# Kernel tuning notes

Hardware: AMD Instinct MI355X
Metric: run time of the kernel (lower is better)

## Reference

```python
import jax, jax.numpy as jnp
import numpy as np

EPS = 1e-12

def _l2norm(v, axis):
    return v / jnp.maximum(jnp.linalg.norm(v, axis=axis, keepdims=True), EPS)

def setup_inputs() -> dict:
    key = jax.random.key(0)
    k1, k2, k3 = jax.random.split(key, 3)
    B, D, C = 65536, 768, 100
    P = C * (C - 1) // 2  # 4950 pairwise local heads
    x = jax.random.normal(k1, (B, D), dtype=jnp.float32)
    first_out = jax.random.normal(k2, (B, C), dtype=jnp.float32)
    weights = jax.random.normal(k3, (P, 2, D), dtype=jnp.float32) * (1.0 / np.sqrt(D))
    sigma = jnp.ones((P,), dtype=jnp.float32)
    return {"x": x, "first_out": first_out, "weights": weights, "sigma": sigma, "cur_stage": 4}

def reference(x, first_out, weights, sigma, cur_stage):
    # top-2 class indices per sample, sorted ascending -> pair key (a, b), a < b
    _, top2 = jax.lax.top_k(first_out, 2)              # [B, 2]
    sorted_idx = jnp.sort(top2, axis=1)                # [B, 2]
    a = sorted_idx[:, 0]
    b = sorted_idx[:, 1]
    pair_idx = b * (b - 1) // 2 + a                    # key 'a-b' -> flat head index
    W = weights[pair_idx]                              # [B, 2, D] gathered expert weights
    s = sigma[pair_idx]                                # [B]
    # CosineLinear (use_RP=False): sigma * normalize(x) @ normalize(W)^T
    xn = _l2norm(x, axis=1)                            # [B, D]
    Wn = _l2norm(W, axis=2)                            # [B, 2, D]
    logits = s[:, None] * jnp.einsum('bd,bkd->bk', xn, Wn)  # [B, 2]
    # pick which of the two candidate classes the local head prefers
    sel = jnp.argmax(logits, axis=1)                   # [B]
    preds = jnp.take_along_axis(sorted_idx, sel[:, None], axis=1)[:, 0]  # [B]
    return preds, logits
```

## Files before the change

### kernel.cpp

```cpp
#include <hip/hip_runtime.h>
#include <math.h>


#define D_DIM 768
#define C_DIM 100
#define EPS_N 1e-12

typedef float vf4 __attribute__((ext_vector_type(4)));

#define ROW_SHR1    0x111
#define ROW_SHR2    0x112
#define ROW_SHR4    0x114
#define ROW_SHR8    0x118
#define ROW_BCAST15 0x142
#define ROW_BCAST31 0x143

template <int CTRL>
__device__ __forceinline__ float dpp0_f32(float v) {
    return __builtin_bit_cast(float, __builtin_amdgcn_update_dpp(
        0, __builtin_bit_cast(int, v), CTRL, 0xF, 0xF, true));
}

template <int CTRL>
__device__ __forceinline__ double dpp0_f64(double v) {
    union { double d; unsigned long long u; } x; x.d = v;
    int lo = (int)(unsigned int)(x.u & 0xffffffffull);
    int hi = (int)(unsigned int)(x.u >> 32);
    int olo = __builtin_amdgcn_update_dpp(0, lo, CTRL, 0xF, 0xF, true);
    int ohi = __builtin_amdgcn_update_dpp(0, hi, CTRL, 0xF, 0xF, true);
    union { unsigned long long u; double d; } y;
    y.u = ((unsigned long long)(unsigned int)ohi << 32) | (unsigned int)olo;
    return y.d;
}

__device__ __forceinline__ float wave_sum_f32(float v) {
    v += dpp0_f32<ROW_SHR1>(v);
    v += dpp0_f32<ROW_SHR2>(v);
    v += dpp0_f32<ROW_SHR4>(v);
    v += dpp0_f32<ROW_SHR8>(v);
    v += dpp0_f32<ROW_BCAST15>(v);
    v += dpp0_f32<ROW_BCAST31>(v);
    return v;
}

__device__ __forceinline__ double wave_sum_f64(double v) {
    v += dpp0_f64<ROW_SHR1>(v);
    v += dpp0_f64<ROW_SHR2>(v);
    v += dpp0_f64<ROW_SHR4>(v);
    v += dpp0_f64<ROW_SHR8>(v);
    v += dpp0_f64<ROW_BCAST15>(v);
    v += dpp0_f64<ROW_BCAST31>(v);
    return v;
}

__device__ __forceinline__ bool vi_gt(float v0, int i0, float v1, int i1) {
    return (v0 > v1) || (v0 == v1 && i0 < i1);
}

template <int CTRL>
__device__ __forceinline__ void t2_step(float& v1, int& i1, float& v2, int& i2) {
    const int NEGINF = 0xFF800000;
    const int BIGIDX = 0x7fffffff;
    float ov1 = __builtin_bit_cast(float, __builtin_amdgcn_update_dpp(
        NEGINF, __builtin_bit_cast(int, v1), CTRL, 0xF, 0xF, false));
    int   oi1 = __builtin_amdgcn_update_dpp(BIGIDX, i1, CTRL, 0xF, 0xF, false);
    float ov2 = __builtin_bit_cast(float, __builtin_amdgcn_update_dpp(
        NEGINF, __builtin_bit_cast(int, v2), CTRL, 0xF, 0xF, false));
    int   oi2 = __builtin_amdgcn_update_dpp(BIGIDX, i2, CTRL, 0xF, 0xF, false);
    if (vi_gt(ov1, oi1, v1, i1)) {
        float nv2; int ni2;
        if (vi_gt(v1, i1, ov2, oi2)) { nv2 = v1;  ni2 = i1; }
        else                         { nv2 = ov2; ni2 = oi2; }
        v1 = ov1; i1 = oi1; v2 = nv2; i2 = ni2;
    } else {
        if (vi_gt(ov1, oi1, v2, i2)) { v2 = ov1; i2 = oi1; }
    }
}

__global__ __launch_bounds__(256) void mlcl_kernel(
    const float* __restrict__ x,
    const float* __restrict__ first_out,
    const float* __restrict__ weights,
    const float* __restrict__ sigma,
    float* __restrict__ out,
    int B)
{
    const int lane = threadIdx.x & 63;
    const int r = (blockIdx.x << 2) + (threadIdx.x >> 6);
    if (r >= B) return;

    const float* fo = first_out + (size_t)r * C_DIM;
    float e0 = fo[lane];
    int   j1 = lane + 64;
    float e1 = (j1 < C_DIM) ? fo[j1] : -INFINITY;

    float v1, v2; int i1, i2;
    if (vi_gt(e1, j1, e0, lane)) { v1 = e1; i1 = j1;   v2 = e0; i2 = lane; }
    else                         { v1 = e0; i1 = lane; v2 = e1; i2 = j1; }

    t2_step<ROW_SHR1>(v1, i1, v2, i2);
    t2_step<ROW_SHR2>(v1, i1, v2, i2);
    t2_step<ROW_SHR4>(v1, i1, v2, i2);
    t2_step<ROW_SHR8>(v1, i1, v2, i2);
    t2_step<ROW_BCAST15>(v1, i1, v2, i2);
    t2_step<ROW_BCAST31>(v1, i1, v2, i2);
    const int gi1 = __builtin_amdgcn_readlane(i1, 63);
    const int gi2 = __builtin_amdgcn_readlane(i2, 63);
    const int a = min(gi1, gi2);
    const int b = max(gi1, gi2);
    const int p = b * (b - 1) / 2 + a;

    const float sig = sigma[p];

    const vf4* xv = (const vf4*)(x + (size_t)r * D_DIM);
    const vf4* wv = (const vf4*)(weights + (size_t)p * (2 * D_DIM));

    vf4 xa0 = xv[lane],       xa1 = xv[lane + 64],       xa2 = xv[lane + 128];
    vf4 w00 = wv[lane],       w01 = wv[lane + 64],       w02 = wv[lane + 128];
    vf4 w10 = wv[192 + lane], w11 = wv[192 + lane + 64], w12 = wv[192 + lane + 128];

    float  xx = 0.f;
    double d0 = 0.0, d1 = 0.0, n0 = 0.0, n1 = 0.0;
#define ACC(xa, w0, w1)                                                       \
    xx += xa.x * xa.x + xa.y * xa.y + xa.z * xa.z + xa.w * xa.w;              \
    d0 += (double)xa.x * w0.x + (double)xa.y * w0.y                           \
        + (double)xa.z * w0.z + (double)xa.w * w0.w;                          \
    d1 += (double)xa.x * w1.x + (double)xa.y * w1.y                           \
        + (double)xa.z * w1.z + (double)xa.w * w1.w;                          \
    n0 += (double)w0.x * w0.x + (double)w0.y * w0.y                           \
        + (double)w0.z * w0.z + (double)w0.w * w0.w;                          \
    n1 += (double)w1.x * w1.x + (double)w1.y * w1.y                           \
        + (double)w1.z * w1.z + (double)w1.w * w1.w;
    ACC(xa0, w00, w10)
    ACC(xa1, w01, w11)
    ACC(xa2, w02, w12)
#undef ACC

    xx = wave_sum_f32(xx);
    d0 = wave_sum_f64(d0);
    d1 = wave_sum_f64(d1);
    n0 = wave_sum_f64(n0);
    n1 = wave_sum_f64(n1);

    if (lane == 63) {
        const double s   = (double)sig;
        const double inx = s / fmax(sqrt((double)xx), EPS_N);
        const double l0  = inx * d0 / fmax(sqrt(n0), EPS_N);
        const double l1  = inx * d1 / fmax(sqrt(n1), EPS_N);
        const int sel = (l1 > l0) ? 1 : 0;
        out[r] = (float)(sel ? b : a);
        float2 lg = make_float2((float)l0, (float)l1);
        *(float2*)(out + B + 2 * (size_t)r) = lg;
    }
}

extern "C" void kernel_launch(void* const* d_in, const int* in_sizes, int n_in,
                              void* d_out, int out_size, void* d_ws, size_t ws_size,
                              hipStream_t stream) {
    const float* x         = (const float*)d_in[0];
    const float* first_out = (const float*)d_in[1];
    const float* weights   = (const float*)d_in[2];
    const float* sigma     = (const float*)d_in[3];
    float* out = (float*)d_out;

    const int B = in_sizes[0] / D_DIM;
    hipLaunchKernelGGL(mlcl_kernel, dim3((B + 3) / 4), dim3(256), 0, stream,
                       x, first_out, weights, sigma, out, B);
}
```

Baseline: 318.4 us.

## Precompute per-head weight inverse norms and process two rows per wavefront

Adds a pre-pass kernel that computes sigma divided by the L2 norm of each of the 9900 weight rows once, in double, and writes the results to workspace. The main kernel then skips the per-sample weight-norm accumulation and reductions and reads two precomputed scalars instead. Each 32-lane half-wave now handles one sample, so reductions are one DPP step shorter, and the x loads are issued before the top-2 search to overlap their latency. The cost is an extra kernel launch and a pass over the weights, plus more registers per lane for the wider per-thread loads.

New measurement: 337.0 us. +5.9%, slower.

```diff
diff --git a/kernel.cpp b/kernel.cpp
--- a/kernel.cpp
+++ b/kernel.cpp
@@ -33,16 +33,22 @@
     return y.d;
 }
 
-__device__ __forceinline__ float wave_sum_f32(float v) {
+__device__ __forceinline__ float half_sum_f32(float v) {
     v += dpp0_f32<ROW_SHR1>(v);
     v += dpp0_f32<ROW_SHR2>(v);
     v += dpp0_f32<ROW_SHR4>(v);
     v += dpp0_f32<ROW_SHR8>(v);
     v += dpp0_f32<ROW_BCAST15>(v);
-    v += dpp0_f32<ROW_BCAST31>(v);
     return v;
 }
-
+__device__ __forceinline__ double half_sum_f64(double v) {
+    v += dpp0_f64<ROW_SHR1>(v);
+    v += dpp0_f64<ROW_SHR2>(v);
+    v += dpp0_f64<ROW_SHR4>(v);
+    v += dpp0_f64<ROW_SHR8>(v);
+    v += dpp0_f64<ROW_BCAST15>(v);
+    return v;
+}
 __device__ __forceinline__ double wave_sum_f64(double v) {
     v += dpp0_f64<ROW_SHR1>(v);
     v += dpp0_f64<ROW_SHR2>(v);
@@ -55,6 +61,12 @@
 
 __device__ __forceinline__ bool vi_gt(float v0, int i0, float v1, int i1) {
     return (v0 > v1) || (v0 == v1 && i0 < i1);
+}
+
+__device__ __forceinline__ void push2(float& v1, int& i1, float& v2, int& i2,
+                                      float v, int i) {
+    if (vi_gt(v, i, v1, i1)) { v2 = v1; i2 = i1; v1 = v; i1 = i; }
+    else if (vi_gt(v, i, v2, i2)) { v2 = v; i2 = i; }
 }
 
 template <int CTRL>
@@ -77,76 +89,112 @@
     }
 }
 
+__global__ __launch_bounds__(256) void norm_kernel(
+    const float* __restrict__ weights,
+    const float* __restrict__ sigma,
+    double* __restrict__ q,
+    int P2)
+{
+    const int lane = threadIdx.x & 63;
+    const int t = (blockIdx.x << 2) + (threadIdx.x >> 6);
+    if (t >= P2) return;
+
+    const vf4* wv = (const vf4*)(weights + (size_t)t * D_DIM);
+    vf4 a0 = wv[lane], a1 = wv[lane + 64], a2 = wv[lane + 128];
+
+    double n = 0.0;
+#define SQ(a)                                                                  \
+    n += (double)a.x * a.x + (double)a.y * a.y                                 \
+       + (double)a.z * a.z + (double)a.w * a.w;
+    SQ(a0) SQ(a1) SQ(a2)
+#undef SQ
+    n = wave_sum_f64(n);
+    if (lane == 63) {
+        q[t] = (double)sigma[t >> 1] / fmax(sqrt(n), EPS_N);
+    }
+}
+
 __global__ __launch_bounds__(256) void mlcl_kernel(
     const float* __restrict__ x,
     const float* __restrict__ first_out,
     const float* __restrict__ weights,
-    const float* __restrict__ sigma,
+    const double* __restrict__ q,
     float* __restrict__ out,
     int B)
 {
     const int lane = threadIdx.x & 63;
-    const int r = (blockIdx.x << 2) + (threadIdx.x >> 6);
+    const int half = lane >> 5;
+    const int hl   = lane & 31;
+    const int r = (blockIdx.x << 3) + ((threadIdx.x >> 6) << 1) + half;
     if (r >= B) return;
 
     const float* fo = first_out + (size_t)r * C_DIM;
-    float e0 = fo[lane];
-    int   j1 = lane + 64;
-    float e1 = (j1 < C_DIM) ? fo[j1] : -INFINITY;
-
-    float v1, v2; int i1, i2;
-    if (vi_gt(e1, j1, e0, lane)) { v1 = e1; i1 = j1;   v2 = e0; i2 = lane; }
-    else                         { v1 = e0; i1 = lane; v2 = e1; i2 = j1; }
+    float c0 = fo[hl];
+    float c1 = fo[hl + 32];
+    float c2 = fo[hl + 64];
+    float c3; int ic3;
+    if (hl + 96 < C_DIM) { c3 = fo[hl + 96]; ic3 = hl + 96; }
+    else                 { c3 = -INFINITY;   ic3 = 0x7fffffff; }
+
+    const vf4* xv = (const vf4*)(x + (size_t)r * D_DIM);
+    vf4 xa0 = xv[hl],       xa1 = xv[hl + 32],  xa2 = xv[hl + 64],
+        xa3 = xv[hl + 96],  xa4 = xv[hl + 128], xa5 = xv[hl + 160];
+
+    float v1 = c0, v2 = -INFINITY;
+    int   i1 = hl, i2 = 0x7fffffff;
+    push2(v1, i1, v2, i2, c1, hl + 32);
+    push2(v1, i1, v2, i2, c2, hl + 64);
+    push2(v1, i1, v2, i2, c3, ic3);
 
     t2_step<ROW_SHR1>(v1, i1, v2, i2);
     t2_step<ROW_SHR2>(v1, i1, v2, i2);
     t2_step<ROW_SHR4>(v1, i1, v2, i2);
     t2_step<ROW_SHR8>(v1, i1, v2, i2);
     t2_step<ROW_BCAST15>(v1, i1, v2, i2);
-    t2_step<ROW_BCAST31>(v1, i1, v2, i2);
-    const int gi1 = __builtin_amdgcn_readlane(i1, 63);
-    const int gi2 = __builtin_amdgcn_readlane(i2, 63);
+    const int i1lo = __builtin_amdgcn_readlane(i1, 31);
+    const int i2lo = __builtin_amdgcn_readlane(i2, 31);
+    const int i1hi = __builtin_amdgcn_readlane(i1, 63);
+    const int i2hi = __builtin_amdgcn_readlane(i2, 63);
+    const int gi1 = half ? i1hi : i1lo;
+    const int gi2 = half ? i2hi : i2lo;
     const int a = min(gi1, gi2);
     const int b = max(gi1, gi2);
     const int p = b * (b - 1) / 2 + a;
 
-    const float sig = sigma[p];
-
-    const vf4* xv = (const vf4*)(x + (size_t)r * D_DIM);
+    const double* qp = q + 2 * (size_t)p;
+    const double q0 = qp[0];
+    const double q1 = qp[1];
+
     const vf4* wv = (const vf4*)(weights + (size_t)p * (2 * D_DIM));
-
-    vf4 xa0 = xv[lane],       xa1 = xv[lane + 64],       xa2 = xv[lane + 128];
-    vf4 w00 = wv[lane],       w01 = wv[lane + 64],       w02 = wv[lane + 128];
-    vf4 w10 = wv[192 + lane], w11 = wv[192 + lane + 64], w12 = wv[192 + lane + 128];
+    vf4 w00 = wv[hl],       w01 = wv[hl + 32],  w02 = wv[hl + 64],
+        w03 = wv[hl + 96],  w04 = wv[hl + 128], w05 = wv[hl + 160];
+    vf4 w10 = wv[192 + hl],       w11 = wv[192 + hl + 32],  w12 = wv[192 + hl + 64],
+        w13 = wv[192 + hl + 96],  w14 = wv[192 + hl + 128], w15 = wv[192 + hl + 160];
 
     float  xx = 0.f;
-    double d0 = 0.0, d1 = 0.0, n0 = 0.0, n1 = 0.0;
+    double d0 = 0.0, d1 = 0.0;
 #define ACC(xa, w0, w1)                                                       \
     xx += xa.x * xa.x + xa.y * xa.y + xa.z * xa.z + xa.w * xa.w;              \
     d0 += (double)xa.x * w0.x + (double)xa.y * w0.y                           \
         + (double)xa.z * w0.z + (double)xa.w * w0.w;                          \
     d1 += (double)xa.x * w1.x + (double)xa.y * w1.y                           \
-        + (double)xa.z * w1.z + (double)xa.w * w1.w;                          \
-    n0 += (double)w0.x * w0.x + (double)w0.y * w0.y                           \
-        + (double)w0.z * w0.z + (double)w0.w * w0.w;                          \
-    n1 += (double)w1.x * w1.x + (double)w1.y * w1.y                           \
-        + (double)w1.z * w1.z + (double)w1.w * w1.w;
+        + (double)xa.z * w1.z + (double)xa.w * w1.w;
     ACC(xa0, w00, w10)
     ACC(xa1, w01, w11)
     ACC(xa2, w02, w12)
+    ACC(xa3, w03, w13)
+    ACC(xa4, w04, w14)
+    ACC(xa5, w05, w15)
 #undef ACC
 
-    xx = wave_sum_f32(xx);
-    d0 = wave_sum_f64(d0);
-    d1 = wave_sum_f64(d1);
-    n0 = wave_sum_f64(n0);
-    n1 = wave_sum_f64(n1);
-
-    if (lane == 63) {
-        const double s   = (double)sig;
-        const double inx = s / fmax(sqrt((double)xx), EPS_N);
-        const double l0  = inx * d0 / fmax(sqrt(n0), EPS_N);
-        const double l1  = inx * d1 / fmax(sqrt(n1), EPS_N);
+    xx = half_sum_f32(xx);
+    d0 = half_sum_f64(d0);
+    d1 = half_sum_f64(d1);
+
+    if (hl == 31) {
+        const double inx = 1.0 / fmax(sqrt((double)xx), EPS_N);
+        const double l0  = q0 * d0 * inx;
+        const double l1  = q1 * d1 * inx;
         const int sel = (l1 > l0) ? 1 : 0;
         out[r] = (float)(sel ? b : a);
         float2 lg = make_float2((float)l0, (float)l1);
@@ -162,8 +210,13 @@
     const float* weights   = (const float*)d_in[2];
     const float* sigma     = (const float*)d_in[3];
     float* out = (float*)d_out;
-
-    const int B = in_sizes[0] / D_DIM;
-    hipLaunchKernelGGL(mlcl_kernel, dim3((B + 3) / 4), dim3(256), 0, stream,
-                       x, first_out, weights, sigma, out, B);
-}
+    double* q  = (double*)d_ws;
+
+    const int B  = in_sizes[0] / D_DIM;
+    const int P2 = in_sizes[2] / D_DIM;
+
+    hipLaunchKernelGGL(norm_kernel, dim3((P2 + 3) / 4), dim3(256), 0, stream,
+                       weights, sigma, q, P2);
+    hipLaunchKernelGGL(mlcl_kernel, dim3((B + 7) / 8), dim3(256), 0, stream,
+                       x, first_out, weights, sigma == nullptr ? nullptr : q, out, B);
+}
```

## Precompute per-head weight norms times sigma in a separate kernel

Applied to the files above, without the earlier changes.

Adds a pre-pass kernel that computes sigma divided by the L2 norm for each of the 9900 weight rows once, in double precision, and stores the results in workspace. The main kernel then reads two doubles instead of recomputing the two weight norms per sample, removing two fp64 dot products and two wave reductions per row. It also issues the x loads before the top-2 selection so they overlap with the reduction. The cost is an extra kernel launch and a full pass over the weights, plus a small dependent load.

Result: no change. 321.4 us (+1.0%).

```diff
diff --git a/kernel.cpp b/kernel.cpp
--- a/kernel.cpp
+++ b/kernel.cpp
@@ -77,11 +77,36 @@
     }
 }
 
+__global__ __launch_bounds__(256) void norm_kernel(
+    const float* __restrict__ weights,
+    const float* __restrict__ sigma,
+    double* __restrict__ q,
+    int P2)
+{
+    const int lane = threadIdx.x & 63;
+    const int t = (blockIdx.x << 2) + (threadIdx.x >> 6);
+    if (t >= P2) return;
+
+    const vf4* wv = (const vf4*)(weights + (size_t)t * D_DIM);
+    vf4 a0 = wv[lane], a1 = wv[lane + 64], a2 = wv[lane + 128];
+
+    double n = 0.0;
+#define SQ(a)                                                                  \
+    n += (double)a.x * a.x + (double)a.y * a.y                                 \
+       + (double)a.z * a.z + (double)a.w * a.w;
+    SQ(a0) SQ(a1) SQ(a2)
+#undef SQ
+    n = wave_sum_f64(n);
+    if (lane == 63) {
+        q[t] = (double)sigma[t >> 1] / fmax(sqrt(n), EPS_N);
+    }
+}
+
 __global__ __launch_bounds__(256) void mlcl_kernel(
     const float* __restrict__ x,
     const float* __restrict__ first_out,
     const float* __restrict__ weights,
-    const float* __restrict__ sigma,
+    const double* __restrict__ q,
     float* __restrict__ out,
     int B)
 {
@@ -93,6 +118,9 @@
     float e0 = fo[lane];
     int   j1 = lane + 64;
     float e1 = (j1 < C_DIM) ? fo[j1] : -INFINITY;
+
+    const vf4* xv = (const vf4*)(x + (size_t)r * D_DIM);
+    vf4 xa0 = xv[lane], xa1 = xv[lane + 64], xa2 = xv[lane + 128];
 
     float v1, v2; int i1, i2;
     if (vi_gt(e1, j1, e0, lane)) { v1 = e1; i1 = j1;   v2 = e0; i2 = lane; }
@@ -110,27 +138,21 @@
     const int b = max(gi1, gi2);
     const int p = b * (b - 1) / 2 + a;
 
-    const float sig = sigma[p];
+    const double q0 = q[2 * (size_t)p];
+    const double q1 = q[2 * (size_t)p + 1];
 
-    const vf4* xv = (const vf4*)(x + (size_t)r * D_DIM);
     const vf4* wv = (const vf4*)(weights + (size_t)p * (2 * D_DIM));
-
-    vf4 xa0 = xv[lane],       xa1 = xv[lane + 64],       xa2 = xv[lane + 128];
     vf4 w00 = wv[lane],       w01 = wv[lane + 64],       w02 = wv[lane + 128];
     vf4 w10 = wv[192 + lane], w11 = wv[192 + lane + 64], w12 = wv[192 + lane + 128];
 
     float  xx = 0.f;
-    double d0 = 0.0, d1 = 0.0, n0 = 0.0, n1 = 0.0;
+    double d0 = 0.0, d1 = 0.0;
 #define ACC(xa, w0, w1)                                                       \
     xx += xa.x * xa.x + xa.y * xa.y + xa.z * xa.z + xa.w * xa.w;              \
     d0 += (double)xa.x * w0.x + (double)xa.y * w0.y                           \
         + (double)xa.z * w0.z + (double)xa.w * w0.w;                          \
     d1 += (double)xa.x * w1.x + (double)xa.y * w1.y                           \
-        + (double)xa.z * w1.z + (double)xa.w * w1.w;                          \
-    n0 += (double)w0.x * w0.x + (double)w0.y * w0.y                           \
-        + (double)w0.z * w0.z + (double)w0.w * w0.w;                          \
-    n1 += (double)w1.x * w1.x + (double)w1.y * w1.y                           \
-        + (double)w1.z * w1.z + (double)w1.w * w1.w;
+        + (double)xa.z * w1.z + (double)xa.w * w1.w;
     ACC(xa0, w00, w10)
     ACC(xa1, w01, w11)
     ACC(xa2, w02, w12)
@@ -139,14 +161,11 @@
     xx = wave_sum_f32(xx);
     d0 = wave_sum_f64(d0);
     d1 = wave_sum_f64(d1);
-    n0 = wave_sum_f64(n0);
-    n1 = wave_sum_f64(n1);
 
     if (lane == 63) {
-        const double s   = (double)sig;
-        const double inx = s / fmax(sqrt((double)xx), EPS_N);
-        const double l0  = inx * d0 / fmax(sqrt(n0), EPS_N);
-        const double l1  = inx * d1 / fmax(sqrt(n1), EPS_N);
+        const double inx = 1.0 / fmax(sqrt((double)xx), EPS_N);
+        const double l0  = q0 * d0 * inx;
+        const double l1  = q1 * d1 * inx;
         const int sel = (l1 > l0) ? 1 : 0;
         out[r] = (float)(sel ? b : a);
         float2 lg = make_float2((float)l0, (float)l1);
@@ -162,8 +181,13 @@
     const float* weights   = (const float*)d_in[2];
     const float* sigma     = (const float*)d_in[3];
     float* out = (float*)d_out;
+    double* q  = (double*)d_ws;
 
-    const int B = in_sizes[0] / D_DIM;
+    const int B  = in_sizes[0] / D_DIM;
+    const int P2 = in_sizes[2] / D_DIM;
+
+    hipLaunchKernelGGL(norm_kernel, dim3((P2 + 3) / 4), dim3(256), 0, stream,
+                       weights, sigma, q, P2);
     hipLaunchKernelGGL(mlcl_kernel, dim3((B + 3) / 4), dim3(256), 0, stream,
-                       x, first_out, weights, sigma, out, B);
+                       x, first_out, weights, q, out, B);
 }
```
